# Performance work log

Hardware: AMD Instinct MI355X
Metric: run time of the kernel (lower is better)

## Reference

```python
import jax, jax.numpy as jnp
import numpy as np
from math import log2, ceil

NUM_LEAVES = 128
KERNEL = 8
STRIDE = 8
PADDING = 0
LR = 0.3

LEAF_NUM = 2 ** ceil(log2(NUM_LEAVES))   # 128
DEPTH = int(log2(LEAF_NUM))              # 7
NUM_NODES = 2 * LEAF_NUM - 1             # 255


def _ancestor_table():
    # A[j-1, t-1] = global heap index of the ancestor of node j at tree level t,
    # or -1 if t exceeds j's own level. Nodes use heap indexing: children of i
    # are 2i+1, 2i+2 (matches the layer bookkeeping in the torch module).
    A = np.full((NUM_NODES - 1, DEPTH), -1, dtype=np.int32)
    for j in range(1, NUM_NODES):
        lvl = int(np.floor(np.log2(j + 1)))
        anc = j
        for t in range(lvl, 0, -1):
            A[j - 1, t - 1] = anc
            anc = (anc - 1) // 2
    return jnp.asarray(A)

_ANC = _ancestor_table()  # (NUM_NODES-1, DEPTH)


def img2patches(x):
    x = jnp.pad(x, PADDING)
    H, W = x.shape
    n0 = (H - KERNEL) // STRIDE + 1
    n1 = (W - KERNEL) // STRIDE + 1
    win = jnp.arange(KERNEL)
    rows = jnp.arange(n0)[:, None] * STRIDE + win[None, :]  # (n0, k)
    cols = jnp.arange(n1)[:, None] * STRIDE + win[None, :]  # (n1, k)
    p = x[rows[:, None, :, None], cols[None, :, None, :]]   # (n0, n1, k, k)
    return p.reshape(n0 * n1, KERNEL * KERNEL)


def setup_inputs() -> dict:
    key = jax.random.key(0)
    k1, k2 = jax.random.split(key)
    image = jax.random.uniform(k1, (2048, 2048), dtype=jnp.float32)
    nodes = jax.random.uniform(k2, (NUM_NODES, KERNEL * KERNEL), dtype=jnp.float32)
    return {"image": image, "nodes": nodes}


def reference(image, nodes):
    X = img2patches(image)                      # (P, k^2)
    P = X.shape[0]

    # --- hierarchical BMU descent (binary tree, DEPTH levels) ---
    cur = jnp.zeros((P,), dtype=jnp.int32)      # root
    bmu_levels = []
    for _ in range(DEPTH):
        c0 = 2 * cur + 1
        c1 = 2 * cur + 2
        # pnorm with p=2 in the source is (sum((a-b)^2))^2 -- monotone, kept faithful
        d0 = jnp.sum((nodes[c0] - X) ** 2, axis=-1) ** 2
        d1 = jnp.sum((nodes[c1] - X) ** 2, axis=-1) ** 2
        cur = jnp.where(d1 < d0, c1, c0)        # tie -> first (c0), like torch.min
        bmu_levels.append(cur)
    bmu_path = jnp.stack(bmu_levels, axis=1)    # (P, DEPTH), bmu at levels 1..DEPTH

    # --- layer_state for every non-root node: number of levels at which the
    # node's ancestor coincides with the BMU chain (== the torch concatenated
    # layer_state, columns ordered by global node index 1..NUM_NODES-1) ---
    state = jnp.sum(_ANC[None, :, :] == bmu_path[:, None, :], axis=-1)  # (P, N-1)

    lrates = LR * (2.0 ** jnp.arange(1, DEPTH + 2, dtype=jnp.float32)) / 2.0 ** (DEPTH + 1)
    lrs = lrates[state]                          # (P, N-1)

    # mean_p lrs[p,j] * (X[p,:] - nodes[1+j,:])
    #   = (lrs^T @ X)/P - mean_p(lrs)[:,None] * nodes[1:]
    upd = jnp.einsum('pj,pk->jk', lrs, X) / P - lrs.mean(axis=0)[:, None] * nodes[1:]
    new_nodes = nodes.at[1:].add(upd)

    return new_nodes, cur[:, None]               # updated codebook, leaf BMU per patch
```

## Files before the change

kernel.cpp:

```cpp
#include <hip/hip_runtime.h>

#define IMG_W 2048
#define NUM_NODES 255
#define NLEAF 128
#define DEPTH 7
#define RS 68

#define A_FLOATS (256 * RS)
#define B_FLOATS (NLEAF * RS)

__global__ __launch_bounds__(1024, 4) void fusedK(const float* __restrict__ img,
                                                  const float* __restrict__ nodes,
                                                  float* __restrict__ leaf_out,
                                                  float* __restrict__ S,
                                                  unsigned* __restrict__ cnt)
{
    __shared__ float smem[A_FLOATS + B_FLOATS];
    __shared__ unsigned cntl[NLEAF];
    __shared__ int Lbuf[256];
    float* nds = smem;
    float* Sl  = smem + A_FLOATS;

    const int t = threadIdx.x;
    const int b = blockIdx.x;

    for (int i = t; i < B_FLOATS; i += 1024) Sl[i] = 0.0f;
    if (t < NLEAF) cntl[t] = 0u;

    const float4* ng = (const float4*)nodes;
    for (int i = t; i < NUM_NODES * 16; i += 1024) {
        *(float4*)&nds[(i >> 4) * RS + (i & 15) * 4] = ng[i];
    }

    const int q = t & 3, g = t >> 2;
    const int p = b * 256 + g;
    const int r = p >> 8, c = p & 255;
    float4 xv0, xv1, xv2, xv3;
    {
        const float* row0 = img + (size_t)(r * 8 + 2 * q) * IMG_W + c * 8;
        xv0 = *(const float4*)(row0);
        xv1 = *(const float4*)(row0 + 4);
        const float* row1 = row0 + IMG_W;
        xv2 = *(const float4*)(row1);
        xv3 = *(const float4*)(row1 + 4);
    }
    __syncthreads();

    int cur = 0;
    #pragma unroll
    for (int lvl = 0; lvl < DEPTH; ++lvl) {
        const int c0 = 2 * cur + 1;
        const float* n0 = &nds[c0 * RS + q * 16];
        const float* n1 = n0 + RS;
        const float4 a0 = *(const float4*)(n0);
        const float4 a1 = *(const float4*)(n0 + 4);
        const float4 a2 = *(const float4*)(n0 + 8);
        const float4 a3 = *(const float4*)(n0 + 12);
        const float4 b0 = *(const float4*)(n1);
        const float4 b1 = *(const float4*)(n1 + 4);
        const float4 b2 = *(const float4*)(n1 + 8);
        const float4 b3 = *(const float4*)(n1 + 12);
        float s0 = 0.f, s1 = 0.f, d;
        d = a0.x - xv0.x; s0 = fmaf(d,d,s0);  d = b0.x - xv0.x; s1 = fmaf(d,d,s1);
        d = a0.y - xv0.y; s0 = fmaf(d,d,s0);  d = b0.y - xv0.y; s1 = fmaf(d,d,s1);
        d = a0.z - xv0.z; s0 = fmaf(d,d,s0);  d = b0.z - xv0.z; s1 = fmaf(d,d,s1);
        d = a0.w - xv0.w; s0 = fmaf(d,d,s0);  d = b0.w - xv0.w; s1 = fmaf(d,d,s1);
        d = a1.x - xv1.x; s0 = fmaf(d,d,s0);  d = b1.x - xv1.x; s1 = fmaf(d,d,s1);
        d = a1.y - xv1.y; s0 = fmaf(d,d,s0);  d = b1.y - xv1.y; s1 = fmaf(d,d,s1);
        d = a1.z - xv1.z; s0 = fmaf(d,d,s0);  d = b1.z - xv1.z; s1 = fmaf(d,d,s1);
        d = a1.w - xv1.w; s0 = fmaf(d,d,s0);  d = b1.w - xv1.w; s1 = fmaf(d,d,s1);
        d = a2.x - xv2.x; s0 = fmaf(d,d,s0);  d = b2.x - xv2.x; s1 = fmaf(d,d,s1);
        d = a2.y - xv2.y; s0 = fmaf(d,d,s0);  d = b2.y - xv2.y; s1 = fmaf(d,d,s1);
        d = a2.z - xv2.z; s0 = fmaf(d,d,s0);  d = b2.z - xv2.z; s1 = fmaf(d,d,s1);
        d = a2.w - xv2.w; s0 = fmaf(d,d,s0);  d = b2.w - xv2.w; s1 = fmaf(d,d,s1);
        d = a3.x - xv3.x; s0 = fmaf(d,d,s0);  d = b3.x - xv3.x; s1 = fmaf(d,d,s1);
        d = a3.y - xv3.y; s0 = fmaf(d,d,s0);  d = b3.y - xv3.y; s1 = fmaf(d,d,s1);
        d = a3.z - xv3.z; s0 = fmaf(d,d,s0);  d = b3.z - xv3.z; s1 = fmaf(d,d,s1);
        d = a3.w - xv3.w; s0 = fmaf(d,d,s0);  d = b3.w - xv3.w; s1 = fmaf(d,d,s1);

        s0 += __shfl_xor(s0, 1); s0 += __shfl_xor(s0, 2);
        s1 += __shfl_xor(s1, 1); s1 += __shfl_xor(s1, 2);

        cur = (s1 < s0) ? (c0 + 1) : c0;
    }
    __syncthreads();

    {
        float* st = &nds[g * RS + q * 16];
        *(float4*)(st)      = xv0;
        *(float4*)(st + 4)  = xv1;
        *(float4*)(st + 8)  = xv2;
        *(float4*)(st + 12) = xv3;
    }
    if (q == 0) {
        const int L = cur - 127;
        Lbuf[g] = L;
        leaf_out[p] = (float)cur;
        atomicAdd(&cntl[L], 1u);
    }
    __syncthreads();

    const int w = t >> 6, k = t & 63;
    for (int i = 0; i < 16; ++i) {
        const int pl = w * 16 + i;
        const int L  = Lbuf[pl];
        atomicAdd(&Sl[L * RS + k], nds[pl * RS + k]);
    }
    __syncthreads();

    for (int i = t; i < NLEAF * 64; i += 1024) {
        const float v = Sl[(i >> 6) * RS + (i & 63)];
        if (v != 0.0f) atomicAdd(&S[i], v);
    }
    if (t < NLEAF && cntl[t] != 0u) atomicAdd(&cnt[t], cntl[t]);
}

__global__ __launch_bounds__(256) void updateK(const float* __restrict__ nodes,
                                               const float* __restrict__ S,
                                               const unsigned* __restrict__ cnt,
                                               float* __restrict__ out)
{
    const int gid = blockIdx.x * 256 + threadIdx.x;
    if (gid >= NUM_NODES * 64) return;
    const int n = gid >> 6, k = gid & 63;
    const float nd = nodes[gid];
    if (n == 0) { out[gid] = nd; return; }

    const int pos = n + 1;
    const int Ln = 31 - __clz(pos);
    float su = 0.f, sc = 0.f;
    #pragma unroll 8
    for (int L = 0; L < NLEAF; ++L) {
        const int a = (128 + L) >> (7 - Ln);
        const int x = pos ^ a;
        const int state = (x == 0) ? Ln : (Ln - (31 - __clz(x)) - 1);
        const float lr = 0.3f * ((float)(1 << state) * (1.0f / 128.0f));
        su = fmaf(lr, S[L * 64 + k], su);
        sc = fmaf(lr, (float)cnt[L], sc);
    }
    const float invP = 1.0f / 65536.0f;
    out[gid] = nd + su * invP - (sc * invP) * nd;
}

extern "C" void kernel_launch(void* const* d_in, const int* in_sizes, int n_in,
                              void* d_out, int out_size, void* d_ws, size_t ws_size,
                              hipStream_t stream)
{
    const float* img   = (const float*)d_in[0];
    const float* nodes = (const float*)d_in[1];

    float* out_nodes = (float*)d_out;
    float* out_leaf  = out_nodes + NUM_NODES * 64;

    float*    S   = (float*)d_ws;
    unsigned* cnt = (unsigned*)(S + NLEAF * 64);

    hipMemsetAsync(d_ws, 0, (NLEAF * 64) * sizeof(float) + NLEAF * sizeof(unsigned), stream);

    fusedK<<<256, 1024, 0, stream>>>(img, nodes, out_leaf, S, cnt);
    updateK<<<64, 256, 0, stream>>>(nodes, S, cnt, out_nodes);
}
```

Measured before the change: 117.7 us.

## Spread each patch across 16 lanes with DPP reductions and direct atomic scatter

Result: faster. 108.8 us (-7.6%).

```diff
diff --git a/kernel.cpp b/kernel.cpp
--- a/kernel.cpp
+++ b/kernel.cpp
@@ -6,8 +6,18 @@
 #define DEPTH 7
 #define RS 68
 
-#define A_FLOATS (256 * RS)
-#define B_FLOATS (NLEAF * RS)
+template<int CTRL>
+__device__ __forceinline__ float dpp_add(float x) {
+    int v = __builtin_amdgcn_update_dpp(0, __float_as_int(x), CTRL, 0xF, 0xF, true);
+    return x + __int_as_float(v);
+}
+__device__ __forceinline__ float group16_sum(float x) {
+    x = dpp_add<0xB1>(x);
+    x = dpp_add<0x4E>(x);
+    x = dpp_add<0x141>(x);
+    x = dpp_add<0x128>(x);
+    return x;
+}
 
 __global__ __launch_bounds__(1024, 4) void fusedK(const float* __restrict__ img,
                                                   const float* __restrict__ nodes,
@@ -15,16 +25,17 @@
                                                   float* __restrict__ S,
                                                   unsigned* __restrict__ cnt)
 {
-    __shared__ float smem[A_FLOATS + B_FLOATS];
+    __shared__ float nds[NUM_NODES * RS];
+    __shared__ float Sl[NLEAF * RS];
     __shared__ unsigned cntl[NLEAF];
-    __shared__ int Lbuf[256];
-    float* nds = smem;
-    float* Sl  = smem + A_FLOATS;
 
     const int t = threadIdx.x;
     const int b = blockIdx.x;
+    const int g = t >> 4;
+    const int q = t & 15;
+    const int q4 = q * 4;
 
-    for (int i = t; i < B_FLOATS; i += 1024) Sl[i] = 0.0f;
+    for (int i = t; i < NLEAF * RS; i += 1024) Sl[i] = 0.0f;
     if (t < NLEAF) cntl[t] = 0u;
 
     const float4* ng = (const float4*)nodes;
@@ -32,79 +43,49 @@
         *(float4*)&nds[(i >> 4) * RS + (i & 15) * 4] = ng[i];
     }
 
-    const int q = t & 3, g = t >> 2;
-    const int p = b * 256 + g;
-    const int r = p >> 8, c = p & 255;
-    float4 xv0, xv1, xv2, xv3;
-    {
-        const float* row0 = img + (size_t)(r * 8 + 2 * q) * IMG_W + c * 8;
-        xv0 = *(const float4*)(row0);
-        xv1 = *(const float4*)(row0 + 4);
-        const float* row1 = row0 + IMG_W;
-        xv2 = *(const float4*)(row1);
-        xv3 = *(const float4*)(row1 + 4);
+    float4 xv[4];
+    #pragma unroll
+    for (int ch = 0; ch < 4; ++ch) {
+        const int p = b * 256 + ch * 64 + g;
+        const int r = p >> 8, c = p & 255;
+        xv[ch] = *(const float4*)(img + (size_t)(r * 8 + (q >> 1)) * IMG_W + c * 8 + (q & 1) * 4);
     }
     __syncthreads();
 
-    int cur = 0;
     #pragma unroll
-    for (int lvl = 0; lvl < DEPTH; ++lvl) {
-        const int c0 = 2 * cur + 1;
-        const float* n0 = &nds[c0 * RS + q * 16];
-        const float* n1 = n0 + RS;
-        const float4 a0 = *(const float4*)(n0);
-        const float4 a1 = *(const float4*)(n0 + 4);
-        const float4 a2 = *(const float4*)(n0 + 8);
-        const float4 a3 = *(const float4*)(n0 + 12);
-        const float4 b0 = *(const float4*)(n1);
-        const float4 b1 = *(const float4*)(n1 + 4);
-        const float4 b2 = *(const float4*)(n1 + 8);
-        const float4 b3 = *(const float4*)(n1 + 12);
-        float s0 = 0.f, s1 = 0.f, d;
-        d = a0.x - xv0.x; s0 = fmaf(d,d,s0);  d = b0.x - xv0.x; s1 = fmaf(d,d,s1);
-        d = a0.y - xv0.y; s0 = fmaf(d,d,s0);  d = b0.y - xv0.y; s1 = fmaf(d,d,s1);
-        d = a0.z - xv0.z; s0 = fmaf(d,d,s0);  d = b0.z - xv0.z; s1 = fmaf(d,d,s1);
-        d = a0.w - xv0.w; s0 = fmaf(d,d,s0);  d = b0.w - xv0.w; s1 = fmaf(d,d,s1);
-        d = a1.x - xv1.x; s0 = fmaf(d,d,s0);  d = b1.x - xv1.x; s1 = fmaf(d,d,s1);
-        d = a1.y - xv1.y; s0 = fmaf(d,d,s0);  d = b1.y - xv1.y; s1 = fmaf(d,d,s1);
-        d = a1.z - xv1.z; s0 = fmaf(d,d,s0);  d = b1.z - xv1.z; s1 = fmaf(d,d,s1);
-        d = a1.w - xv1.w; s0 = fmaf(d,d,s0);  d = b1.w - xv1.w; s1 = fmaf(d,d,s1);
-        d = a2.x - xv2.x; s0 = fmaf(d,d,s0);  d = b2.x - xv2.x; s1 = fmaf(d,d,s1);
-        d = a2.y - xv2.y; s0 = fmaf(d,d,s0);  d = b2.y - xv2.y; s1 = fmaf(d,d,s1);
-        d = a2.z - xv2.z; s0 = fmaf(d,d,s0);  d = b2.z - xv2.z; s1 = fmaf(d,d,s1);
-        d = a2.w - xv2.w; s0 = fmaf(d,d,s0);  d = b2.w - xv2.w; s1 = fmaf(d,d,s1);
-        d = a3.x - xv3.x; s0 = fmaf(d,d,s0);  d = b3.x - xv3.x; s1 = fmaf(d,d,s1);
-        d = a3.y - xv3.y; s0 = fmaf(d,d,s0);  d = b3.y - xv3.y; s1 = fmaf(d,d,s1);
-        d = a3.z - xv3.z; s0 = fmaf(d,d,s0);  d = b3.z - xv3.z; s1 = fmaf(d,d,s1);
-        d = a3.w - xv3.w; s0 = fmaf(d,d,s0);  d = b3.w - xv3.w; s1 = fmaf(d,d,s1);
+    for (int ch = 0; ch < 4; ++ch) {
+        const float4 x = xv[ch];
+        int cur = 0;
+        #pragma unroll
+        for (int lvl = 0; lvl < DEPTH; ++lvl) {
+            const int c0 = 2 * cur + 1;
+            const float* base = &nds[c0 * RS + q4];
+            const float4 a  = *(const float4*)(base);
+            const float4 bb = *(const float4*)(base + RS);
+            float s0 = 0.f, s1 = 0.f, d;
+            d = a.x  - x.x; s0 = fmaf(d, d, s0);
+            d = a.y  - x.y; s0 = fmaf(d, d, s0);
+            d = a.z  - x.z; s0 = fmaf(d, d, s0);
+            d = a.w  - x.w; s0 = fmaf(d, d, s0);
+            d = bb.x - x.x; s1 = fmaf(d, d, s1);
+            d = bb.y - x.y; s1 = fmaf(d, d, s1);
+            d = bb.z - x.z; s1 = fmaf(d, d, s1);
+            d = bb.w - x.w; s1 = fmaf(d, d, s1);
+            s0 = group16_sum(s0);
+            s1 = group16_sum(s1);
+            cur = (s1 < s0) ? (c0 + 1) : c0;
+        }
 
-        s0 += __shfl_xor(s0, 1); s0 += __shfl_xor(s0, 2);
-        s1 += __shfl_xor(s1, 1); s1 += __shfl_xor(s1, 2);
-
-        cur = (s1 < s0) ? (c0 + 1) : c0;
-    }
-    __syncthreads();
-
-    {
-        float* st = &nds[g * RS + q * 16];
-        *(float4*)(st)      = xv0;
-        *(float4*)(st + 4)  = xv1;
-        *(float4*)(st + 8)  = xv2;
-        *(float4*)(st + 12) = xv3;
-    }
-    if (q == 0) {
         const int L = cur - 127;
-        Lbuf[g] = L;
-        leaf_out[p] = (float)cur;
-        atomicAdd(&cntl[L], 1u);
-    }
-    __syncthreads();
-
-    const int w = t >> 6, k = t & 63;
-    for (int i = 0; i < 16; ++i) {
-        const int pl = w * 16 + i;
-        const int L  = Lbuf[pl];
-        atomicAdd(&Sl[L * RS + k], nds[pl * RS + k]);
+        if (q == 0) {
+            leaf_out[b * 256 + ch * 64 + g] = (float)cur;
+            atomicAdd(&cntl[L], 1u);
+        }
+        float* dst = &Sl[L * RS + q4];
+        atomicAdd(dst + 0, x.x);
+        atomicAdd(dst + 1, x.y);
+        atomicAdd(dst + 2, x.z);
+        atomicAdd(dst + 3, x.w);
     }
     __syncthreads();
 
@@ -156,7 +137,6 @@
     unsigned* cnt = (unsigned*)(S + NLEAF * 64);
 
     hipMemsetAsync(d_ws, 0, (NLEAF * 64) * sizeof(float) + NLEAF * sizeof(unsigned), stream);
-
     fusedK<<<256, 1024, 0, stream>>>(img, nodes, out_leaf, S, cnt);
     updateK<<<64, 256, 0, stream>>>(nodes, S, cnt, out_nodes);
 }
```
